# Kernel optimization log

Hardware: AMD Instinct MI355X
Metric: run time of the kernel (lower is better)

## Reference

```python
import jax, jax.numpy as jnp
import numpy as np

# config (from UnifiedAttentionConfig defaults)
D = 512; H = 8; C = 64; DQ = 256; NI = 2; CI = 64
TOPK = 32; LMAX = 16; NWIN = 128; ROPE_BASE = 10000.0
B = 1; T = 1024; LP = 8; P = T // LP
NEG = -1e30


def _rope_cache(seq_len, dim):
    half = dim // 2
    inv = 1.0 / (ROPE_BASE ** (jnp.arange(half, dtype=jnp.float32) / half))
    f = jnp.arange(seq_len, dtype=jnp.float32)[:, None] * inv[None, :]
    emb = jnp.concatenate([f, f], axis=-1)
    return jnp.cos(emb), jnp.sin(emb)


def _rot(x, cos, sin):
    half = x.shape[-1] // 2
    x1, x2 = x[..., :half], x[..., half:]
    return x * cos + jnp.concatenate([-x2, x1], axis=-1) * sin


def _rms(x, w, eps=1e-6):
    return x * jax.lax.rsqrt(jnp.mean(x * x, axis=-1, keepdims=True) + eps) * w


def _forward(h, W_dq, W_uq, W_csa_kv, W_csa_z, B_csa, W_idx_kv, W_idx_z, B_idx,
             W_iuq, W_w, W_swkv, qnorm_w, knorm_w, W_o, sink_logits,
             phrase_mask, phrase_token_idx, phrase_end_pos):
    Bq, Tq, Dq = h.shape
    Pn, Lmax = phrase_mask.shape[1], phrase_mask.shape[2]
    scale = 1.0 / jnp.sqrt(jnp.float32(C))
    cos, sin = _rope_cache(Tq, C)
    cos_i, sin_i = _rope_cache(Tq, CI)
    # ---- queries: compress -> up-project -> RMSNorm -> RoPE (per-token) ----
    q_lat = h @ W_dq                                      # (B,T,DQ)
    q = (q_lat @ W_uq).reshape(Bq, Tq, H, C)
    q = _rot(_rms(q, qnorm_w), cos[:, None, :], sin[:, None, :])
    # ---- gather phrase tokens ----
    idx = phrase_token_idx.reshape(Bq, Pn * Lmax)
    hp = jnp.take_along_axis(h, idx[:, :, None], axis=1).reshape(Bq, Pn, Lmax, Dq)
    m = phrase_mask                                       # (B,P,Lmax) bool
    # ---- multi-head phrase compression (CSA KV) ----
    c_tok = (hp @ W_csa_kv).reshape(Bq, Pn, Lmax, H, C)
    z = (hp @ W_csa_z).reshape(Bq, Pn, Lmax, H, C) + B_csa[None, None]
    z = jnp.where(m[..., None, None], z, NEG)
    g = jax.nn.softmax(z, axis=2)
    g = jnp.where(m.any(axis=2)[:, :, None, None, None], g, 0.0)
    c_csa = jnp.sum(g * c_tok, axis=2)                    # (B,P,H,C) values
    pos = jnp.clip(phrase_end_pos, 0, Tq - 1)
    k_csa = _rot(_rms(c_csa, knorm_w), cos[pos][:, :, None, :], sin[pos][:, :, None, :])
    # ---- single-head phrase compression (indexer keys) ----
    ck = hp @ W_idx_kv                                    # (B,P,Lmax,CI)
    zk = hp @ W_idx_z + B_idx[None, None]
    zk = jnp.where(m[..., None], zk, NEG)
    gk = jax.nn.softmax(zk, axis=2)
    gk = jnp.where(m.any(axis=2)[:, :, None, None], gk, 0.0)
    k_idx = jnp.sum(gk * ck, axis=2)                      # (B,P,CI)
    k_idx = _rot(k_idx, cos_i[pos], sin_i[pos])
    # ---- lightning indexer + causal top-k routing ----
    q_i = (q_lat @ W_iuq).reshape(Bq, Tq, NI, CI)
    s = jax.nn.relu(jnp.einsum('bthd,bpd->bthp', q_i, k_idx))
    I = jnp.sum(s * (h @ W_w)[..., None], axis=2)         # (B,T,P)
    t_idx = jnp.arange(Tq)
    valid = (phrase_end_pos[:, None, :] <= t_idx[None, :, None]) & (phrase_end_pos[:, None, :] >= 0)
    I = jnp.where(valid, I, NEG)
    vals, sel = jax.lax.top_k(I, TOPK)                    # (B,T,K)
    sel_ok = vals > NEG * 0.5
    k_sel = jnp.take_along_axis(k_csa[:, None], sel[:, :, :, None, None], axis=2)  # (B,T,K,H,C)
    v_sel = jnp.take_along_axis(c_csa[:, None], sel[:, :, :, None, None], axis=2)
    logit_csa = jnp.einsum('bthc,btkhc->bthk', q, k_sel) * scale
    logit_csa = jnp.where(sel_ok[:, :, None, :], logit_csa, NEG)
    # ---- sliding window (fixed mode) ----
    kv = (h @ W_swkv).reshape(Bq, Tq, H, C)
    k_sw = _rot(_rms(kv, knorm_w), cos[:, None, :], sin[:, None, :])
    widx = t_idx[:, None] + jnp.arange(NWIN)[None, :] - (NWIN - 1)  # (T,W)
    w_ok = widx >= 0
    widx_c = jnp.clip(widx, 0, Tq - 1)
    k_win = k_sw[:, widx_c]                               # (B,T,W,H,C)
    v_win = kv[:, widx_c]
    logit_sw = jnp.einsum('bthc,btwhc->bthw', q, k_win) * scale
    logit_sw = jnp.where(w_ok[None, :, None, :], logit_sw, NEG)
    # ---- single softmax over [csa | window | sink] ----
    sink = jnp.broadcast_to(sink_logits.reshape(1, 1, H, 1), (Bq, Tq, H, 1))
    pattn = jax.nn.softmax(jnp.concatenate([logit_csa, logit_sw, sink], axis=-1), axis=-1)
    out = jnp.einsum('bthk,btkhc->bthc', pattn[..., :TOPK], v_sel) \
        + jnp.einsum('bthw,btwhc->bthc', pattn[..., TOPK:TOPK + NWIN], v_win)
    return out.reshape(Bq, Tq, H * C) @ W_o


def setup_inputs() -> dict:
    key = jax.random.key(0)
    ks = jax.random.split(key, 16)
    nrm = lambda k, shp: 0.02 * jax.random.normal(k, shp, dtype=jnp.float32)
    # structured phrases: phrase p covers tokens [p*LP, p*LP+LP), padded to LMAX
    l = np.arange(LMAX)
    mask = np.broadcast_to(l < LP, (B, P, LMAX)).copy()
    tok = np.minimum(l, LP - 1)[None, :] + (np.arange(P) * LP)[:, None]
    tok = np.broadcast_to(tok, (B, P, LMAX)).copy()
    end = np.broadcast_to(np.arange(P) * LP + LP - 1, (B, P)).copy()
    pid = np.broadcast_to(np.arange(T) // LP, (B, T)).copy()
    return {
        'h': jax.random.normal(ks[0], (B, T, D), dtype=jnp.float32),
        'phrase_mask': jnp.asarray(mask, dtype=bool),
        'phrase_token_idx': jnp.asarray(tok, dtype=jnp.int32),
        'phrase_end_pos': jnp.asarray(end, dtype=jnp.int32),
        'phrase_id': jnp.asarray(pid, dtype=jnp.int32),
        'W_dq': nrm(ks[1], (D, DQ)),
        'W_uq': nrm(ks[2], (DQ, H * C)),
        'W_csa_kv': nrm(ks[3], (D, H * C)),
        'W_csa_z': nrm(ks[4], (D, H * C)),
        'B_csa': nrm(ks[5], (LMAX, H, C)),
        'W_idx_kv': nrm(ks[6], (D, CI)),
        'W_idx_z': nrm(ks[7], (D, CI)),
        'B_idx': nrm(ks[8], (LMAX, CI)),
        'W_iuq': nrm(ks[9], (DQ, NI * CI)),
        'W_w': nrm(ks[10], (D, NI)),
        'W_swkv': nrm(ks[11], (D, H * C)),
        'qnorm_w': jnp.ones((C,), dtype=jnp.float32),
        'knorm_w': jnp.ones((C,), dtype=jnp.float32),
        'W_o': nrm(ks[12], (H * C, D)),
        'sink_logits': nrm(ks[13], (H,)),
    }


def reference(h, phrase_mask, phrase_token_idx, phrase_end_pos, phrase_id,
              W_dq, W_uq, W_csa_kv, W_csa_z, B_csa, W_idx_kv, W_idx_z, B_idx,
              W_iuq, W_w, W_swkv, qnorm_w, knorm_w, W_o, sink_logits):
    del phrase_id  # only used when sw_mode == 'phrase'
    return _forward(h, W_dq, W_uq, W_csa_kv, W_csa_z, B_csa, W_idx_kv, W_idx_z,
                    B_idx, W_iuq, W_w, W_swkv, qnorm_w, knorm_w, W_o, sink_logits,
                    phrase_mask, phrase_token_idx, phrase_end_pos)
```

## Files before the change

kernel.cpp:

```cpp
#include <hip/hip_runtime.h>
#include <cmath>

static constexpr int Tn = 1024, Dn = 512, Hn = 8, Cn = 64, DQn = 256,
                     NIn = 2, CIn = 64, TK = 32, LM = 16, NW = 128, Pn = 128;
#define NEGV (-1e30f)

typedef unsigned short u16;
typedef __bf16 bf16x8 __attribute__((ext_vector_type(8)));
typedef float f32x4 __attribute__((ext_vector_type(4)));

__device__ __forceinline__ u16 f2bf(float x) {
  unsigned u = __float_as_uint(x);
  return (u16)((u + 0x7fffu + ((u >> 16) & 1u)) >> 16);
}
__device__ __forceinline__ float bf2f(u16 b) {
  return __uint_as_float((unsigned)b << 16);
}

struct PackJobs {
  const float* src[7];
  u16* dst[7];
  int start[8];
  int N[7];
  int logN[7];
  int isA[7];
  int ps[7];
};

__global__ __launch_bounds__(256) void pack_all(PackJobs pj) {
  int i = blockIdx.x * 256 + threadIdx.x;
  if (i >= pj.start[7]) return;
  int j = 0;
  while (i >= pj.start[j + 1]) ++j;
  int local = i - pj.start[j];
  const float* s = pj.src[j];
  u16* dh = pj.dst[j];
  u16* dl = dh + pj.ps[j];
  float x[8];
  size_t idx;
  if (pj.isA[j]) {
    int m = local & 1023;
    int kg = local >> 10;
    const float4* p = reinterpret_cast<const float4*>(s + (size_t)m * 512 + kg * 8);
    float4 a = p[0], b = p[1];
    x[0] = a.x; x[1] = a.y; x[2] = a.z; x[3] = a.w;
    x[4] = b.x; x[5] = b.y; x[6] = b.z; x[7] = b.w;
    idx = ((size_t)kg * 1024 + m) * 8;
  } else {
    int N = pj.N[j];
    int n = local & (N - 1);
    int kg = local >> pj.logN[j];
#pragma unroll
    for (int e = 0; e < 8; ++e) x[e] = s[(size_t)(kg * 8 + e) * N + n];
    idx = ((size_t)kg * N + n) * 8;
  }
  union { u16 u[8]; int4 v; } oh, ol;
#pragma unroll
  for (int e = 0; e < 8; ++e) {
    u16 hb = f2bf(x[e]);
    oh.u[e] = hb;
    ol.u[e] = f2bf(x[e] - bf2f(hb));
  }
  *reinterpret_cast<int4*>(dh + idx) = oh.v;
  *reinterpret_cast<int4*>(dl + idx) = ol.v;
}

struct TileDesc {
  const u16* Blo;
  const u16* Bhi;
  float* Clo;
  float* Chi;
  u16* Cp;
  int ldNlo, ldNhi, ldClo, ldChi, mode, n0, bps, cpps;
};
struct GemmArgs {
  TileDesc d[15];
};

#define GLD16(gp, lp)                                                     \
  __builtin_amdgcn_global_load_lds(                                      \
      (const __attribute__((address_space(1))) unsigned int*)(gp),       \
      (__attribute__((address_space(3))) unsigned int*)(lp), 16, 0, 0)

template <int FMW>
__global__ __launch_bounds__(256) void gemm_bf16(const u16* __restrict__ Ap,
                                                 int NK, int aps, GemmArgs ga) {
  constexpr int MT = FMW * 32;
  const int ct = blockIdx.x, rt = blockIdx.y;
  const TileDesc d = ga.d[ct];
  const int m0 = rt * MT;
  __shared__ __align__(16) u16 lA[2][2][4][MT][8];
  __shared__ __align__(16) u16 lB[2][2][4][128][8];
  const int tid = threadIdx.x;
  const int w = tid >> 6, lane = tid & 63;
  const int wm = w >> 1, wn = w & 1;

  f32x4 acc[FMW][4];
#pragma unroll
  for (int a = 0; a < FMW; ++a)
#pragma unroll
    for (int b = 0; b < 4; ++b)
#pragma unroll
      for (int r = 0; r < 4; ++r) acc[a][b][r] = 0.f;

  auto stage = [&](int buf, int kg) {
#pragma unroll
    for (int r0 = 0; r0 < MT; r0 += 64) {
      GLD16(Ap + ((size_t)kg * 1024 + m0 + r0 + lane) * 8, &lA[buf][0][w][r0][0]);
      GLD16(Ap + aps + ((size_t)kg * 1024 + m0 + r0 + lane) * 8, &lA[buf][1][w][r0][0]);
    }
    GLD16(d.Blo + ((size_t)kg * d.ldNlo + lane) * 8, &lB[buf][0][w][0][0]);
    GLD16(d.Bhi + ((size_t)kg * d.ldNhi + lane) * 8, &lB[buf][0][w][64][0]);
    GLD16(d.Blo + d.bps + ((size_t)kg * d.ldNlo + lane) * 8, &lB[buf][1][w][0][0]);
    GLD16(d.Bhi + d.bps + ((size_t)kg * d.ldNhi + lane) * 8, &lB[buf][1][w][64][0]);
  };

  stage(0, w);
  const int kq = lane >> 4, fr = lane & 15;
  for (int ks = 0; ks < NK; ++ks) {
    __syncthreads();
    if (ks + 1 < NK) stage((ks + 1) & 1, (ks + 1) * 4 + w);
    const int cb = ks & 1;
    bf16x8 aFh[FMW], aFl[FMW], bFh[4], bFl[4];
#pragma unroll
    for (int f = 0; f < FMW; ++f) {
      aFh[f] = *reinterpret_cast<const bf16x8*>(&lA[cb][0][kq][wm * (FMW * 16) + f * 16 + fr][0]);
      aFl[f] = *reinterpret_cast<const bf16x8*>(&lA[cb][1][kq][wm * (FMW * 16) + f * 16 + fr][0]);
    }
#pragma unroll
    for (int f = 0; f < 4; ++f) {
      bFh[f] = *reinterpret_cast<const bf16x8*>(&lB[cb][0][kq][wn * 64 + f * 16 + fr][0]);
      bFl[f] = *reinterpret_cast<const bf16x8*>(&lB[cb][1][kq][wn * 64 + f * 16 + fr][0]);
    }
#pragma unroll
    for (int fm = 0; fm < FMW; ++fm)
#pragma unroll
      for (int fn = 0; fn < 4; ++fn) {
        acc[fm][fn] = __builtin_amdgcn_mfma_f32_16x16x32_bf16(aFh[fm], bFh[fn],
                                                              acc[fm][fn], 0, 0, 0);
        acc[fm][fn] = __builtin_amdgcn_mfma_f32_16x16x32_bf16(aFl[fm], bFh[fn],
                                                              acc[fm][fn], 0, 0, 0);
        acc[fm][fn] = __builtin_amdgcn_mfma_f32_16x16x32_bf16(aFh[fm], bFl[fn],
                                                              acc[fm][fn], 0, 0, 0);
      }
  }
  float* Cb = (wn == 0) ? d.Clo : d.Chi;
  const int ldc = (wn == 0) ? d.ldClo : d.ldChi;
  if (d.mode != 1) {
#pragma unroll
    for (int fm = 0; fm < FMW; ++fm)
#pragma unroll
      for (int fn = 0; fn < 4; ++fn)
#pragma unroll
        for (int r = 0; r < 4; ++r) {
          int row = m0 + wm * (FMW * 16) + fm * 16 + (lane >> 4) * 4 + r;
          int cl = fn * 16 + fr;
          Cb[(size_t)row * ldc + cl] = acc[fm][fn][r];
        }
  }
  if (d.mode >= 1) {
#pragma unroll
    for (int fm = 0; fm < FMW; ++fm)
#pragma unroll
      for (int fn = 0; fn < 4; ++fn)
#pragma unroll
        for (int r = 0; r < 4; ++r) {
          int row = m0 + wm * (FMW * 16) + fm * 16 + (lane >> 4) * 4 + r;
          int gc = d.n0 + wn * 64 + fn * 16 + fr;
          float v = acc[fm][fn][r];
          u16 hb = f2bf(v);
          u16 lb = f2bf(v - bf2f(hb));
          size_t idx = ((size_t)(gc >> 3) * 1024 + row) * 8 + (gc & 7);
          d.Cp[idx] = hb;
          d.Cp[idx + d.cpps] = lb;
        }
  }
}

__global__ __launch_bounds__(256) void idx_kernel(
    const float* __restrict__ h, const float* __restrict__ q_lat,
    const float* __restrict__ Wikv, const float* __restrict__ Wiz,
    const float* __restrict__ Wiuq, float* __restrict__ hikv,
    float* __restrict__ hiz, float* __restrict__ qib) {
  const int t0 = blockIdx.x * 4;
  const int tid = threadIdx.x;
  __shared__ float hs[4][Dn];
  __shared__ float ql[4][DQn];
  for (int i = tid; i < 4 * Dn; i += 256)
    hs[i >> 9][i & 511] = h[(size_t)(t0 + (i >> 9)) * Dn + (i & 511)];
  for (int i = tid; i < 4 * DQn; i += 256)
    ql[i >> 8][i & 255] = q_lat[(size_t)(t0 + (i >> 8)) * DQn + (i & 255)];
  __syncthreads();
  if (tid < 128) {
    const float* Wm = (tid < 64) ? Wikv : Wiz;
    const int ci = tid & 63;
    float a0 = 0.f, a1 = 0.f, a2 = 0.f, a3 = 0.f;
#pragma unroll 8
    for (int k = 0; k < Dn; ++k) {
      float wv = Wm[k * CIn + ci];
      a0 += hs[0][k] * wv;
      a1 += hs[1][k] * wv;
      a2 += hs[2][k] * wv;
      a3 += hs[3][k] * wv;
    }
    float* dst = (tid < 64) ? hikv : hiz;
    dst[(size_t)(t0 + 0) * CIn + ci] = a0;
    dst[(size_t)(t0 + 1) * CIn + ci] = a1;
    dst[(size_t)(t0 + 2) * CIn + ci] = a2;
    dst[(size_t)(t0 + 3) * CIn + ci] = a3;
  } else {
    const int jj = tid - 128;
    float a0 = 0.f, a1 = 0.f, a2 = 0.f, a3 = 0.f;
#pragma unroll 8
    for (int k = 0; k < DQn; ++k) {
      float wv = Wiuq[k * 128 + jj];
      a0 += ql[0][k] * wv;
      a1 += ql[1][k] * wv;
      a2 += ql[2][k] * wv;
      a3 += ql[3][k] * wv;
    }
    qib[(size_t)(t0 + 0) * 128 + jj] = a0;
    qib[(size_t)(t0 + 1) * 128 + jj] = a1;
    qib[(size_t)(t0 + 2) * 128 + jj] = a2;
    qib[(size_t)(t0 + 3) * 128 + jj] = a3;
  }
}

__global__ __launch_bounds__(512) void phrase_rope_kernel(
    const int* __restrict__ maskbuf, const int* __restrict__ tokbuf,
    const int* __restrict__ endbuf, const float* __restrict__ hckv,
    const float* __restrict__ hcz, const float* __restrict__ hikv,
    const float* __restrict__ hiz, const float* __restrict__ Bcsa,
    const float* __restrict__ Bidx, const float* __restrict__ knw,
    const float* __restrict__ qnw, float* __restrict__ ccsa,
    float* __restrict__ kcsa, float* __restrict__ kidx,
    float* __restrict__ q, const float* __restrict__ kv,
    float* __restrict__ ksw) {
  const int tid = threadIdx.x;
  const int c = tid & 63;
  const float sgn = (c < 32) ? -1.f : 1.f;

  if (blockIdx.x >= Pn) {
    const int t = blockIdx.x - Pn;
    const float fr = (float)t * powf(10000.0f, -(float)(c & 31) / 32.0f);
    const float cv = cosf(fr), sv = sinf(fr);
    {
      float x = q[t * Dn + tid];
      float ss = x * x;
#pragma unroll
      for (int off = 32; off; off >>= 1) ss += __shfl_xor(ss, off, 64);
      float xr = x * rsqrtf(ss / (float)Cn + 1e-6f) * qnw[c];
      float pr = __shfl_xor(xr, 32, 64);
      q[t * Dn + tid] = xr * cv + sgn * pr * sv;
    }
    {
      float y = kv[t * Dn + tid];
      float ss = y * y;
#pragma unroll
      for (int off = 32; off; off >>= 1) ss += __shfl_xor(ss, off, 64);
      float yr = y * rsqrtf(ss / (float)Cn + 1e-6f) * knw[c];
      float pr = __shfl_xor(yr, 32, 64);
      ksw[t * Dn + tid] = yr * cv + sgn * pr * sv;
    }
    return;
  }

  const int p = blockIdx.x;
  __shared__ int s_bytemode;
  __shared__ int s_tok[LM];
  __shared__ int s_m[LM];
  __shared__ int s_pos, s_anyv;

  if (tid == 0) s_bytemode = 0;
  __syncthreads();
  {
    unsigned wv = ((const unsigned*)maskbuf)[tid];
    if (wv > 1u) atomicOr(&s_bytemode, 1);
  }
  __syncthreads();
  const int bytemode = s_bytemode;
  if (tid < LM) {
    int mv;
    if (bytemode)
      mv = ((const unsigned char*)maskbuf)[p * LM + tid] != 0;
    else
      mv = maskbuf[p * LM + tid] != 0;
    s_m[tid] = mv;
    s_tok[tid] = tokbuf[p * LM + tid];
  }
  if (tid == 0) {
    int e = endbuf[p];
    s_pos = min(max(e, 0), Tn - 1);
  }
  __syncthreads();
  if (tid == 0) {
    int any = 0;
    for (int l = 0; l < LM; ++l) any |= s_m[l];
    s_anyv = any;
  }
  __syncthreads();
  const int anyv = s_anyv;
  const int pos = s_pos;
  const float fr = (float)pos * powf(10000.0f, -(float)(c & 31) / 32.0f);
  const float cv = cosf(fr), sv = sinf(fr);

  {
    float z[LM];
    float zmax = NEGV;
#pragma unroll
    for (int l = 0; l < LM; ++l) {
      float zv = hcz[s_tok[l] * Dn + tid] + Bcsa[l * (Hn * Cn) + tid];
      zv = s_m[l] ? zv : NEGV;
      z[l] = zv;
      zmax = fmaxf(zmax, zv);
    }
    float den = 0.f, num = 0.f;
#pragma unroll
    for (int l = 0; l < LM; ++l) {
      float e = expf(z[l] - zmax);
      den += e;
      num += e * hckv[s_tok[l] * Dn + tid];
    }
    float cc = anyv ? (num / den) : 0.f;
    ccsa[p * (Hn * Cn) + tid] = cc;

    float ss = cc * cc;
#pragma unroll
    for (int off = 32; off; off >>= 1) ss += __shfl_xor(ss, off, 64);
    float kn = cc * rsqrtf(ss / (float)Cn + 1e-6f) * knw[c];
    float pr = __shfl_xor(kn, 32, 64);
    kcsa[p * (Hn * Cn) + tid] = kn * cv + sgn * pr * sv;
  }

  if (tid < CIn) {
    float zk[LM];
    float zm = NEGV;
#pragma unroll
    for (int l = 0; l < LM; ++l) {
      float zv = hiz[s_tok[l] * CIn + tid] + Bidx[l * CIn + tid];
      zv = s_m[l] ? zv : NEGV;
      zk[l] = zv;
      zm = fmaxf(zm, zv);
    }
    float dk = 0.f, nk = 0.f;
#pragma unroll
    for (int l = 0; l < LM; ++l) {
      float e = expf(zk[l] - zm);
      dk += e;
      nk += e * hikv[s_tok[l] * CIn + tid];
    }
    float ki = anyv ? (nk / dk) : 0.f;
    float pr = __shfl_xor(ki, 32, 64);
    kidx[p * CIn + tid] = ki * cv + sgn * pr * sv;
  }
}

__global__ __launch_bounds__(128) void score_topk_kernel(
    const float* __restrict__ hbuf, const float* __restrict__ Ww,
    const float* __restrict__ qi, const float* __restrict__ kidx,
    const int* __restrict__ endbuf, int* __restrict__ sel,
    int* __restrict__ selok) {
  const int t = blockIdx.x;
  const int tid = threadIdx.x;
  __shared__ float sqi[NIn * CIn];
  __shared__ float kT[CIn][Pn + 1];
  __shared__ float sI[Pn];
  __shared__ float sp0[128], sp1[128];

  sqi[tid] = qi[(size_t)t * (NIn * CIn) + tid];
#pragma unroll
  for (int it = 0; it < 16; ++it) {
    int idx4 = it * 128 + tid;
    float4 v = reinterpret_cast<const float4*>(kidx)[idx4];
    int p = idx4 >> 4;
    int c4 = (idx4 & 15) * 4;
    kT[c4 + 0][p] = v.x;
    kT[c4 + 1][p] = v.y;
    kT[c4 + 2][p] = v.z;
    kT[c4 + 3][p] = v.w;
  }
  float p0 = 0.f, p1 = 0.f;
#pragma unroll
  for (int e4 = 0; e4 < 4; ++e4) {
    int e = tid * 4 + e4;
    float hv = hbuf[(size_t)t * Dn + e];
    p0 += hv * Ww[e * NIn + 0];
    p1 += hv * Ww[e * NIn + 1];
  }
  sp0[tid] = p0;
  sp1[tid] = p1;
  __syncthreads();
  for (int srd = 64; srd; srd >>= 1) {
    if (tid < srd) {
      sp0[tid] += sp0[tid + srd];
      sp1[tid] += sp1[tid + srd];
    }
    __syncthreads();
  }
  const float ww0 = sp0[0], ww1 = sp1[0];

  {
    const int p = tid;
    float s0 = 0.f, s1 = 0.f;
#pragma unroll 16
    for (int ci = 0; ci < CIn; ++ci) {
      float kc = kT[ci][p];
      s0 += sqi[ci] * kc;
      s1 += sqi[CIn + ci] * kc;
    }
    float Iv = fmaxf(s0, 0.f) * ww0 + fmaxf(s1, 0.f) * ww1;
    int e = endbuf[p];
    if (!(e <= t && e >= 0)) Iv = NEGV;
    sI[p] = Iv;
  }
  __syncthreads();

  if (tid < 64) {
    float v0 = sI[tid], v1 = sI[tid + 64];
    for (int it = 0; it < TK; ++it) {
      float bv;
      int bi;
      if (v0 >= v1) { bv = v0; bi = tid; } else { bv = v1; bi = tid + 64; }
#pragma unroll
      for (int off = 32; off; off >>= 1) {
        float ov = __shfl_xor(bv, off, 64);
        int oi = __shfl_xor(bi, off, 64);
        if (ov > bv || (ov == bv && oi < bi)) { bv = ov; bi = oi; }
      }
      if (tid == 0) {
        sel[t * TK + it] = bi;
        selok[t * TK + it] = (bv > NEGV * 0.5f) ? 1 : 0;
      }
      if (bi == tid) v0 = -3.4e38f;
      if (bi == tid + 64) v1 = -3.4e38f;
    }
  }
}

__global__ __launch_bounds__(256) void attn4_kernel(
    const float* __restrict__ q, const float* __restrict__ ksw,
    const float* __restrict__ kv, const float* __restrict__ kcsa,
    const float* __restrict__ ccsa, const int* __restrict__ sel,
    const int* __restrict__ selok, const float* __restrict__ sink,
    u16* __restrict__ atp) {
  const int tid = threadIdx.x;
  const int wid = tid >> 6, lane = tid & 63;
  const int g = lane >> 4;
  const int gl = lane & 15;
  const int h = blockIdx.x >> 8;
  const int t = ((blockIdx.x & 255) << 2) + wid;

  __shared__ float slog[4][164];
  __shared__ int s_sel[4][TK];
  __shared__ int s_ok[4][TK];

  if (lane < TK) {
    s_sel[wid][lane] = sel[t * TK + lane];
    s_ok[wid][lane] = selok[t * TK + lane];
  }
  const int hc = h * Cn + gl * 4;
  const float4 qf = *reinterpret_cast<const float4*>(&q[t * Dn + hc]);
  float* myslog = slog[wid];

#pragma unroll 4
  for (int pass = 0; pass < 32; ++pass) {
    int w = pass * 4 + g;
    int src = t + w - (NW - 1);
    int srcc = max(src, 0);
    float4 kk = *reinterpret_cast<const float4*>(&ksw[srcc * Dn + hc]);
    float acc = qf.x * kk.x + qf.y * kk.y + qf.z * kk.z + qf.w * kk.w;
#pragma unroll
    for (int off = 1; off < 16; off <<= 1) acc += __shfl_xor(acc, off, 64);
    if (gl == 0) myslog[TK + w] = (src >= 0) ? acc * 0.125f : NEGV;
  }
#pragma unroll 2
  for (int pass = 0; pass < 8; ++pass) {
    int s = pass * 4 + g;
    int se = s_sel[wid][s];
    float4 kk = *reinterpret_cast<const float4*>(&kcsa[se * Dn + hc]);
    float acc = qf.x * kk.x + qf.y * kk.y + qf.z * kk.z + qf.w * kk.w;
#pragma unroll
    for (int off = 1; off < 16; off <<= 1) acc += __shfl_xor(acc, off, 64);
    if (gl == 0) myslog[s] = s_ok[wid][s] ? acc * 0.125f : NEGV;
  }
  if (lane == 0) myslog[160] = sink[h];

  float x0 = myslog[lane];
  float x1 = myslog[lane + 64];
  float x2 = (lane < 33) ? myslog[lane + 128] : NEGV;
  float m = fmaxf(x0, fmaxf(x1, x2));
#pragma unroll
  for (int off = 32; off; off >>= 1) m = fmaxf(m, __shfl_xor(m, off, 64));
  float e0 = expf(x0 - m), e1 = expf(x1 - m);
  float e2 = (lane < 33) ? expf(x2 - m) : 0.f;
  float sden = e0 + e1 + e2;
#pragma unroll
  for (int off = 32; off; off >>= 1) sden += __shfl_xor(sden, off, 64);
  const float inv = 1.f / sden;
  myslog[lane] = e0 * inv;
  myslog[lane + 64] = e1 * inv;
  if (lane < 33) myslog[lane + 128] = e2 * inv;

  float4 acc = make_float4(0.f, 0.f, 0.f, 0.f);
#pragma unroll 4
  for (int pass = 0; pass < 32; ++pass) {
    int w = pass * 4 + g;
    int src = t + w - (NW - 1);
    int srcc = max(src, 0);
    float pv = myslog[TK + w];
    pv = (src >= 0) ? pv : 0.f;
    float4 vv = *reinterpret_cast<const float4*>(&kv[srcc * Dn + hc]);
    acc.x += pv * vv.x;
    acc.y += pv * vv.y;
    acc.z += pv * vv.z;
    acc.w += pv * vv.w;
  }
#pragma unroll 2
  for (int pass = 0; pass < 8; ++pass) {
    int s = pass * 4 + g;
    float pv = myslog[s];
    int se = s_sel[wid][s];
    float4 vv = *reinterpret_cast<const float4*>(&ccsa[se * Dn + hc]);
    acc.x += pv * vv.x;
    acc.y += pv * vv.y;
    acc.z += pv * vv.z;
    acc.w += pv * vv.w;
  }
  acc.x += __shfl_xor(acc.x, 16, 64);
  acc.y += __shfl_xor(acc.y, 16, 64);
  acc.z += __shfl_xor(acc.z, 16, 64);
  acc.w += __shfl_xor(acc.w, 16, 64);
  acc.x += __shfl_xor(acc.x, 32, 64);
  acc.y += __shfl_xor(acc.y, 32, 64);
  acc.z += __shfl_xor(acc.z, 32, 64);
  acc.w += __shfl_xor(acc.w, 32, 64);
  if (lane < 16) {
    float vals[4] = {acc.x, acc.y, acc.z, acc.w};
    int colb = h * Cn + lane * 4;
#pragma unroll
    for (int r = 0; r < 4; ++r) {
      int gc = colb + r;
      float v = vals[r];
      u16 hb = f2bf(v);
      u16 lb = f2bf(v - bf2f(hb));
      size_t idx = ((size_t)(gc >> 3) * 1024 + t) * 8 + (gc & 7);
      atp[idx] = hb;
      atp[idx + 524288] = lb;
    }
  }
}

extern "C" void kernel_launch(void* const* d_in, const int* in_sizes, int n_in,
                              void* d_out, int out_size, void* d_ws,
                              size_t ws_size, hipStream_t stream) {
  const float* h = (const float*)d_in[0];
  const int* mask = (const int*)d_in[1];
  const int* tok = (const int*)d_in[2];
  const int* endp = (const int*)d_in[3];
  const float* W_dq = (const float*)d_in[5];
  const float* W_uq = (const float*)d_in[6];
  const float* W_csa_kv = (const float*)d_in[7];
  const float* W_csa_z = (const float*)d_in[8];
  const float* B_csa = (const float*)d_in[9];
  const float* W_idx_kv = (const float*)d_in[10];
  const float* W_idx_z = (const float*)d_in[11];
  const float* B_idx = (const float*)d_in[12];
  const float* W_iuq = (const float*)d_in[13];
  const float* W_w = (const float*)d_in[14];
  const float* W_swkv = (const float*)d_in[15];
  const float* qnw = (const float*)d_in[16];
  const float* knw = (const float*)d_in[17];
  const float* W_o = (const float*)d_in[18];
  const float* sink = (const float*)d_in[19];

  float* ws = (float*)d_ws;
  u16* hA = (u16*)(ws + 0);
  float* qbuf = ws + 0;
  u16* qlP = (u16*)(ws + 524288);
  float* hckv = ws + 786432;
  u16* atP = (u16*)(ws + 786432);
  float* hcz = ws + 1310720;
  float* kvb = ws + 1835008;
  float* hikv = ws + 2359296;
  float* hiz = ws + 2424832;
  float* q_lat = ws + 2490368;
  float* ccsa = ws + 2752512;
  float* kcsa = ws + 2818048;
  float* kidx = ws + 2883584;
  int* seli = (int*)(ws + 2891776);
  int* selok = (int*)(ws + 2924544);
  float* qib = ws + 2957312;
  float* kswb = ws + 3088384;
  u16* pW = (u16*)(ws + 3612672);
  u16* pWdq = pW;
  u16* pWckv = pW + 262144;
  u16* pWcz = pW + 786432;
  u16* pWsw = pW + 1310720;
  u16* pWuq = pW + 1835008;
  u16* pWo = pW + 2097152;
  float* outp = (float*)d_out;

  {
    PackJobs pj{};
    const float* srcs[7] = {h, W_dq, W_csa_kv, W_csa_z, W_swkv, W_uq, W_o};
    u16* dsts[7] = {hA, pWdq, pWckv, pWcz, pWsw, pWuq, pWo};
    int Ns[7] = {0, 256, 512, 512, 512, 512, 512};
    int logNs[7] = {0, 8, 9, 9, 9, 9, 9};
    int Ks[7] = {512, 512, 512, 512, 512, 256, 512};
    int isA[7] = {1, 0, 0, 0, 0, 0, 0};
    int pss[7] = {524288, 131072, 262144, 262144, 262144, 131072, 262144};
    int s = 0;
    for (int i = 0; i < 7; ++i) {
      pj.src[i] = srcs[i];
      pj.dst[i] = dsts[i];
      pj.N[i] = Ns[i];
      pj.logN[i] = logNs[i];
      pj.isA[i] = isA[i];
      pj.ps[i] = pss[i];
      pj.start[i] = s;
      s += isA[i] ? 1024 * (Ks[i] / 8) : (Ks[i] / 8) * Ns[i];
    }
    pj.start[7] = s;
    pack_all<<<(s + 255) / 256, 256, 0, stream>>>(pj);
  }

  auto normTile = [](const u16* pB, int N, int n0, float* C, int ldc, int bps) {
    TileDesc td{};
    td.Blo = pB + n0 * 8;
    td.Bhi = pB + (n0 + 64) * 8;
    td.ldNlo = td.ldNhi = N;
    td.Clo = C + n0;
    td.Chi = C + n0 + 64;
    td.ldClo = td.ldChi = ldc;
    td.mode = 0;
    td.bps = bps;
    return td;
  };

  {
    GemmArgs ga{};
    int nt = 0;
    for (int n0 = 0; n0 < 256; n0 += 128) {
      TileDesc td = normTile(pWdq, 256, n0, q_lat, 256, 131072);
      td.mode = 2;
      td.Cp = qlP;
      td.cpps = 262144;
      td.n0 = n0;
      ga.d[nt++] = td;
    }
    for (int n0 = 0; n0 < 512; n0 += 128) ga.d[nt++] = normTile(pWckv, 512, n0, hckv, 512, 262144);
    for (int n0 = 0; n0 < 512; n0 += 128) ga.d[nt++] = normTile(pWcz, 512, n0, hcz, 512, 262144);
    for (int n0 = 0; n0 < 512; n0 += 128) ga.d[nt++] = normTile(pWsw, 512, n0, kvb, 512, 262144);
    gemm_bf16<2><<<dim3(nt, 16), 256, 0, stream>>>(hA, 16, 524288, ga);
  }
  {
    GemmArgs ga{};
    int nt = 0;
    for (int n0 = 0; n0 < 512; n0 += 128) ga.d[nt++] = normTile(pWuq, 512, n0, qbuf, 512, 131072);
    gemm_bf16<2><<<dim3(nt, 16), 256, 0, stream>>>(qlP, 8, 262144, ga);
  }
  idx_kernel<<<Tn / 4, 256, 0, stream>>>(h, q_lat, W_idx_kv, W_idx_z, W_iuq,
                                         hikv, hiz, qib);
  phrase_rope_kernel<<<Pn + Tn, 512, 0, stream>>>(
      mask, tok, endp, hckv, hcz, hikv, hiz, B_csa, B_idx, knw, qnw, ccsa,
      kcsa, kidx, qbuf, kvb, kswb);
  score_topk_kernel<<<Tn, 128, 0, stream>>>(h, W_w, qib, kidx, endp, seli,
                                            selok);
  attn4_kernel<<<dim3(Tn / 4 * Hn), 256, 0, stream>>>(qbuf, kswb, kvb, kcsa,
                                                      ccsa, seli, selok, sink,
                                                      atP);
  {
    GemmArgs ga{};
    int nt = 0;
    for (int n0 = 0; n0 < 512; n0 += 128) ga.d[nt++] = normTile(pWo, 512, n0, outp, 512, 262144);
    gemm_bf16<2><<<dim3(nt, 16), 256, 0, stream>>>(atP, 16, 524288, ga);
  }
  (void)in_sizes; (void)n_in; (void)out_size; (void)ws_size;
}
```

Baseline: 136.6 us.

## Replace LDS-staged GEMM with direct-load per-wave GEMM, fuse up-proj into idx kernel

Replaces the LDS double-buffered GEMM with a kernel in which each wave loads its A/B fragments straight from global memory and computes a 32x64 tile. This removes the shared-memory staging and block-level barriers, and splits the output into more, smaller tiles. The W_uq up-projection GEMM is merged into the indexer projection kernel as extra leading blocks, which saves one launch. The attention kernel is widened from 4 to 8 tokens per 512-thread block. Direct global loads lose the data reuse that LDS provided and may raise memory traffic.

```diff
diff --git a/kernel.cpp b/kernel.cpp
--- a/kernel.cpp
+++ b/kernel.cpp
@@ -65,75 +65,50 @@
   *reinterpret_cast<int4*>(dl + idx) = ol.v;
 }
 
-struct TileDesc {
-  const u16* Blo;
-  const u16* Bhi;
-  float* Clo;
-  float* Chi;
+struct WDesc {
+  const u16* B;
+  float* C;
   u16* Cp;
-  int ldNlo, ldNhi, ldClo, ldChi, mode, n0, bps, cpps;
+  int ldN, ldC, mode, n0g, bps, cpps;
 };
-struct GemmArgs {
-  TileDesc d[15];
+struct WArgs {
+  WDesc d[28];
 };
 
-#define GLD16(gp, lp)                                                     \
-  __builtin_amdgcn_global_load_lds(                                      \
-      (const __attribute__((address_space(1))) unsigned int*)(gp),       \
-      (__attribute__((address_space(3))) unsigned int*)(lp), 16, 0, 0)
-
-template <int FMW>
-__global__ __launch_bounds__(256) void gemm_bf16(const u16* __restrict__ Ap,
-                                                 int NK, int aps, GemmArgs ga) {
-  constexpr int MT = FMW * 32;
-  const int ct = blockIdx.x, rt = blockIdx.y;
-  const TileDesc d = ga.d[ct];
-  const int m0 = rt * MT;
-  __shared__ __align__(16) u16 lA[2][2][4][MT][8];
-  __shared__ __align__(16) u16 lB[2][2][4][128][8];
-  const int tid = threadIdx.x;
-  const int w = tid >> 6, lane = tid & 63;
-  const int wm = w >> 1, wn = w & 1;
-
-  f32x4 acc[FMW][4];
-#pragma unroll
-  for (int a = 0; a < FMW; ++a)
+__global__ __launch_bounds__(256) void gemm_direct(const u16* __restrict__ Ap,
+                                                   int aps, int NK, WArgs wa) {
+  const int lane = threadIdx.x & 63;
+  const int wid = (blockIdx.x * 256 + threadIdx.x) >> 6;
+  const int nt = wid >> 5, mt = wid & 31;
+  const WDesc d = wa.d[nt];
+  const int m0 = mt * 32;
+  const int kq = lane >> 4, fr = lane & 15;
+
+  f32x4 acc[2][4];
+#pragma unroll
+  for (int a = 0; a < 2; ++a)
 #pragma unroll
     for (int b = 0; b < 4; ++b)
 #pragma unroll
       for (int r = 0; r < 4; ++r) acc[a][b][r] = 0.f;
 
-  auto stage = [&](int buf, int kg) {
-#pragma unroll
-    for (int r0 = 0; r0 < MT; r0 += 64) {
-      GLD16(Ap + ((size_t)kg * 1024 + m0 + r0 + lane) * 8, &lA[buf][0][w][r0][0]);
-      GLD16(Ap + aps + ((size_t)kg * 1024 + m0 + r0 + lane) * 8, &lA[buf][1][w][r0][0]);
-    }
-    GLD16(d.Blo + ((size_t)kg * d.ldNlo + lane) * 8, &lB[buf][0][w][0][0]);
-    GLD16(d.Bhi + ((size_t)kg * d.ldNhi + lane) * 8, &lB[buf][0][w][64][0]);
-    GLD16(d.Blo + d.bps + ((size_t)kg * d.ldNlo + lane) * 8, &lB[buf][1][w][0][0]);
-    GLD16(d.Bhi + d.bps + ((size_t)kg * d.ldNhi + lane) * 8, &lB[buf][1][w][64][0]);
-  };
-
-  stage(0, w);
-  const int kq = lane >> 4, fr = lane & 15;
+#pragma unroll 2
   for (int ks = 0; ks < NK; ++ks) {
-    __syncthreads();
-    if (ks + 1 < NK) stage((ks + 1) & 1, (ks + 1) * 4 + w);
-    const int cb = ks & 1;
-    bf16x8 aFh[FMW], aFl[FMW], bFh[4], bFl[4];
-#pragma unroll
-    for (int f = 0; f < FMW; ++f) {
-      aFh[f] = *reinterpret_cast<const bf16x8*>(&lA[cb][0][kq][wm * (FMW * 16) + f * 16 + fr][0]);
-      aFl[f] = *reinterpret_cast<const bf16x8*>(&lA[cb][1][kq][wm * (FMW * 16) + f * 16 + fr][0]);
-    }
+    const int kg = ks * 4 + kq;
+    const size_t ab = ((size_t)kg * 1024 + m0 + fr) * 8;
+    bf16x8 aFh[2], aFl[2], bFh[4], bFl[4];
+    aFh[0] = *reinterpret_cast<const bf16x8*>(Ap + ab);
+    aFh[1] = *reinterpret_cast<const bf16x8*>(Ap + ab + 128);
+    aFl[0] = *reinterpret_cast<const bf16x8*>(Ap + aps + ab);
+    aFl[1] = *reinterpret_cast<const bf16x8*>(Ap + aps + ab + 128);
+    const size_t bb = ((size_t)kg * d.ldN + fr) * 8;
 #pragma unroll
     for (int f = 0; f < 4; ++f) {
-      bFh[f] = *reinterpret_cast<const bf16x8*>(&lB[cb][0][kq][wn * 64 + f * 16 + fr][0]);
-      bFl[f] = *reinterpret_cast<const bf16x8*>(&lB[cb][1][kq][wn * 64 + f * 16 + fr][0]);
-    }
-#pragma unroll
-    for (int fm = 0; fm < FMW; ++fm)
+      bFh[f] = *reinterpret_cast<const bf16x8*>(d.B + bb + f * 128);
+      bFl[f] = *reinterpret_cast<const bf16x8*>(d.B + d.bps + bb + f * 128);
+    }
+#pragma unroll
+    for (int fm = 0; fm < 2; ++fm)
 #pragma unroll
       for (int fn = 0; fn < 4; ++fn) {
         acc[fm][fn] = __builtin_amdgcn_mfma_f32_16x16x32_bf16(aFh[fm], bFh[fn],
@@ -144,29 +119,26 @@
                                                               acc[fm][fn], 0, 0, 0);
       }
   }
-  float* Cb = (wn == 0) ? d.Clo : d.Chi;
-  const int ldc = (wn == 0) ? d.ldClo : d.ldChi;
   if (d.mode != 1) {
 #pragma unroll
-    for (int fm = 0; fm < FMW; ++fm)
+    for (int fm = 0; fm < 2; ++fm)
 #pragma unroll
       for (int fn = 0; fn < 4; ++fn)
 #pragma unroll
         for (int r = 0; r < 4; ++r) {
-          int row = m0 + wm * (FMW * 16) + fm * 16 + (lane >> 4) * 4 + r;
-          int cl = fn * 16 + fr;
-          Cb[(size_t)row * ldc + cl] = acc[fm][fn][r];
+          int row = m0 + fm * 16 + kq * 4 + r;
+          d.C[(size_t)row * d.ldC + fn * 16 + fr] = acc[fm][fn][r];
         }
   }
   if (d.mode >= 1) {
 #pragma unroll
-    for (int fm = 0; fm < FMW; ++fm)
+    for (int fm = 0; fm < 2; ++fm)
 #pragma unroll
       for (int fn = 0; fn < 4; ++fn)
 #pragma unroll
         for (int r = 0; r < 4; ++r) {
-          int row = m0 + wm * (FMW * 16) + fm * 16 + (lane >> 4) * 4 + r;
-          int gc = d.n0 + wn * 64 + fn * 16 + fr;
+          int row = m0 + fm * 16 + kq * 4 + r;
+          int gc = d.n0g + fn * 16 + fr;
           float v = acc[fm][fn][r];
           u16 hb = f2bf(v);
           u16 lb = f2bf(v - bf2f(hb));
@@ -177,15 +149,73 @@
   }
 }
 
-__global__ __launch_bounds__(256) void idx_kernel(
+__global__ __launch_bounds__(256) void k2idx_kernel(
+    const u16* __restrict__ Ap, int aps, WArgs wa,
     const float* __restrict__ h, const float* __restrict__ q_lat,
     const float* __restrict__ Wikv, const float* __restrict__ Wiz,
     const float* __restrict__ Wiuq, float* __restrict__ hikv,
     float* __restrict__ hiz, float* __restrict__ qib) {
-  const int t0 = blockIdx.x * 4;
+  const int bid = blockIdx.x;
   const int tid = threadIdx.x;
+
+  if (bid < 64) {
+    const int lane = tid & 63;
+    const int wid = (bid * 256 + tid) >> 6;
+    const int nt = wid >> 5, mt = wid & 31;
+    const WDesc d = wa.d[nt];
+    const int m0 = mt * 32;
+    const int kq = lane >> 4, fr = lane & 15;
+
+    f32x4 acc[2][4];
+#pragma unroll
+    for (int a = 0; a < 2; ++a)
+#pragma unroll
+      for (int b = 0; b < 4; ++b)
+#pragma unroll
+        for (int r = 0; r < 4; ++r) acc[a][b][r] = 0.f;
+
+#pragma unroll 2
+    for (int ks = 0; ks < 8; ++ks) {
+      const int kg = ks * 4 + kq;
+      const size_t ab = ((size_t)kg * 1024 + m0 + fr) * 8;
+      bf16x8 aFh[2], aFl[2], bFh[4], bFl[4];
+      aFh[0] = *reinterpret_cast<const bf16x8*>(Ap + ab);
+      aFh[1] = *reinterpret_cast<const bf16x8*>(Ap + ab + 128);
+      aFl[0] = *reinterpret_cast<const bf16x8*>(Ap + aps + ab);
+      aFl[1] = *reinterpret_cast<const bf16x8*>(Ap + aps + ab + 128);
+      const size_t bb = ((size_t)kg * d.ldN + fr) * 8;
+#pragma unroll
+      for (int f = 0; f < 4; ++f) {
+        bFh[f] = *reinterpret_cast<const bf16x8*>(d.B + bb + f * 128);
+        bFl[f] = *reinterpret_cast<const bf16x8*>(d.B + d.bps + bb + f * 128);
+      }
+#pragma unroll
+      for (int fm = 0; fm < 2; ++fm)
+#pragma unroll
+        for (int fn = 0; fn < 4; ++fn) {
+          acc[fm][fn] = __builtin_amdgcn_mfma_f32_16x16x32_bf16(aFh[fm], bFh[fn],
+                                                                acc[fm][fn], 0, 0, 0);
+          acc[fm][fn] = __builtin_amdgcn_mfma_f32_16x16x32_bf16(aFl[fm], bFh[fn],
+                                                                acc[fm][fn], 0, 0, 0);
+          acc[fm][fn] = __builtin_amdgcn_mfma_f32_16x16x32_bf16(aFh[fm], bFl[fn],
+                                                                acc[fm][fn], 0, 0, 0);
+        }
+    }
+#pragma unroll
+    for (int fm = 0; fm < 2; ++fm)
+#pragma unroll
+      for (int fn = 0; fn < 4; ++fn)
+#pragma unroll
+        for (int r = 0; r < 4; ++r) {
+          int row = m0 + fm * 16 + kq * 4 + r;
+          d.C[(size_t)row * d.ldC + fn * 16 + fr] = acc[fm][fn][r];
+        }
+    return;
+  }
+
   __shared__ float hs[4][Dn];
   __shared__ float ql[4][DQn];
+  const int t0 = (bid - 64) * 4;
   for (int i = tid; i < 4 * Dn; i += 256)
     hs[i >> 9][i & 511] = h[(size_t)(t0 + (i >> 9)) * Dn + (i & 511)];
   for (int i = tid; i < 4 * DQn; i += 256)
@@ -437,7 +467,7 @@
   }
 }
 
-__global__ __launch_bounds__(256) void attn4_kernel(
+__global__ __launch_bounds__(512) void attn8_kernel(
     const float* __restrict__ q, const float* __restrict__ ksw,
     const float* __restrict__ kv, const float* __restrict__ kcsa,
     const float* __restrict__ ccsa, const int* __restrict__ sel,
@@ -447,12 +477,12 @@
   const int wid = tid >> 6, lane = tid & 63;
   const int g = lane >> 4;
   const int gl = lane & 15;
-  const int h = blockIdx.x >> 8;
-  const int t = ((blockIdx.x & 255) << 2) + wid;
-
-  __shared__ float slog[4][164];
-  __shared__ int s_sel[4][TK];
-  __shared__ int s_ok[4][TK];
+  const int h = blockIdx.x >> 7;
+  const int t = ((blockIdx.x & 127) << 3) + wid;
+
+  __shared__ float slog[8][164];
+  __shared__ int s_sel[8][TK];
+  __shared__ int s_ok[8][TK];
 
   if (lane < TK) {
     s_sel[wid][lane] = sel[t * TK + lane];
@@ -624,56 +654,54 @@
     pack_all<<<(s + 255) / 256, 256, 0, stream>>>(pj);
   }
 
-  auto normTile = [](const u16* pB, int N, int n0, float* C, int ldc, int bps) {
-    TileDesc td{};
-    td.Blo = pB + n0 * 8;
-    td.Bhi = pB + (n0 + 64) * 8;
-    td.ldNlo = td.ldNhi = N;
-    td.Clo = C + n0;
-    td.Chi = C + n0 + 64;
-    td.ldClo = td.ldChi = ldc;
-    td.mode = 0;
-    td.bps = bps;
-    return td;
+  auto mkDesc = [](const u16* pB, int N, int n0, float* C, int ldc, int bps) {
+    WDesc d{};
+    d.B = pB + n0 * 8;
+    d.C = C + n0;
+    d.ldN = N;
+    d.ldC = ldc;
+    d.mode = 0;
+    d.n0g = n0;
+    d.bps = bps;
+    return d;
   };
 
   {
-    GemmArgs ga{};
+    WArgs wa{};
     int nt = 0;
-    for (int n0 = 0; n0 < 256; n0 += 128) {
-      TileDesc td = normTile(pWdq, 256, n0, q_lat, 256, 131072);
-      td.mode = 2;
-      td.Cp = qlP;
-      td.cpps = 262144;
-      td.n0 = n0;
-      ga.d[nt++] = td;
-    }
-    for (int n0 = 0; n0 < 512; n0 += 128) ga.d[nt++] = normTile(pWckv, 512, n0, hckv, 512, 262144);
-    for (int n0 = 0; n0 < 512; n0 += 128) ga.d[nt++] = normTile(pWcz, 512, n0, hcz, 512, 262144);
-    for (int n0 = 0; n0 < 512; n0 += 128) ga.d[nt++] = normTile(pWsw, 512, n0, kvb, 512, 262144);
-    gemm_bf16<2><<<dim3(nt, 16), 256, 0, stream>>>(hA, 16, 524288, ga);
+    for (int n0 = 0; n0 < 256; n0 += 64) {
+      WDesc d = mkDesc(pWdq, 256, n0, q_lat, 256, 131072);
+      d.mode = 2;
+      d.Cp = qlP;
+      d.cpps = 262144;
+      wa.d[nt++] = d;
+    }
+    for (int n0 = 0; n0 < 512; n0 += 64) wa.d[nt++] = mkDesc(pWckv, 512, n0, hckv, 512, 262144);
+    for (int n0 = 0; n0 < 512; n0 += 64) wa.d[nt++] = mkDesc(pWcz, 512, n0, hcz, 512, 262144);
+    for (int n0 = 0; n0 < 512; n0 += 64) wa.d[nt++] = mkDesc(pWsw, 512, n0, kvb, 512, 262144);
+    gemm_direct<<<nt * 32 / 4, 256, 0, stream>>>(hA, 524288, 16, wa);
   }
   {
-    GemmArgs ga{};
+    WArgs wa{};
     int nt = 0;
-    for (int n0 = 0; n0 < 512; n0 += 128) ga.d[nt++] = normTile(pWuq, 512, n0, qbuf, 512, 131072);
-    gemm_bf16<2><<<dim3(nt, 16), 256, 0, stream>>>(qlP, 8, 262144, ga);
-  }
-  idx_kernel<<<Tn / 4, 256, 0, stream>>>(h, q_lat, W_idx_kv, W_idx_z, W_iuq,
-                                         hikv, hiz, qib);
+    for (int n0 = 0; n0 < 512; n0 += 64) wa.d[nt++] = mkDesc(pWuq, 512, n0, qbuf, 512, 131072);
+    k2idx_kernel<<<64 + Tn / 4, 256, 0, stream>>>(qlP, 262144, wa, h, q_lat,
+                                                  W_idx_kv, W_idx_z, W_iuq,
+                                                  hikv, hiz, qib);
+  }
   phrase_rope_kernel<<<Pn + Tn, 512, 0, stream>>>(
       mask, tok, endp, hckv, hcz, hikv, hiz, B_csa, B_idx, knw, qnw, ccsa,
       kcsa, kidx, qbuf, kvb, kswb);
   score_topk_kernel<<<Tn, 128, 0, stream>>>(h, W_w, qib, kidx, endp, seli,
                                             selok);
-  attn4_kernel<<<dim3(Tn / 4 * Hn), 256, 0, stream>>>(qbuf, kswb, kvb, kcsa,
+  attn8_kernel<<<dim3(Tn / 8 * Hn), 512, 0, stream>>>(qbuf, kswb, kvb, kcsa,
                                                       ccsa, seli, selok, sink,
                                                       atP);
   {
-    GemmArgs ga{};
+    WArgs wa{};
     int nt = 0;
-    for (int n0 = 0; n0 < 512; n0 += 128) ga.d[nt++] = normTile(pWo, 512, n0, outp, 512, 262144);
-    gemm_bf16<2><<<dim3(nt, 16), 256, 0, stream>>>(atP, 16, 524288, ga);
+    for (int n0 = 0; n0 < 512; n0 += 64) wa.d[nt++] = mkDesc(pWo, 512, n0, outp, 512, 262144);
+    gemm_direct<<<nt * 32 / 4, 256, 0, stream>>>(atP, 524288, 16, wa);
   }
   (void)in_sizes; (void)n_in; (void)out_size; (void)ws_size;
 }
```

Result: faster. 130.4 us (-4.5%).
